# Performance work log

Hardware: AMD Instinct MI355X
Metric: run time of the kernel (lower is better)

## Reference

```python
import jax, jax.numpy as jnp
import numpy as np

N = 131072; B = 4; PER = N // B
M = 32768; MPER = M // B; K = 16; E = M * K
NF = 16; C = 32
BNC = float(1.0 / np.sqrt(1.0 + 1e-5))  # BatchNorm1d in eval mode, default running stats (mean=0,var=1,affine=identity)
_kd = np.array([[1.,1.,1.],[-1.,1.,1.],[1.,-1.,1.],[1.,1.,-1.],[-1.,-1.,1.],[-1.,1.,-1.],[1.,-1.,-1.],[-1.,-1.,-1.]], np.float32) / np.float32(np.sqrt(3.0))
KDIRS = jnp.asarray(_kd)  # [8,3] LightKernel directions


def _ln(x, g, b):
    m = x.mean(-1, keepdims=True)
    v = ((x - m) ** 2).mean(-1, keepdims=True)
    return (x - m) / jnp.sqrt(v + 1e-5) * g + b


def _mlp2(x, w1, b1, w2, b2):
    # Seq(Lin, BN, SiLU) x2 ; BN in eval mode == multiply by BNC
    h = jax.nn.silu(BNC * (x @ w1 + b1))
    return jax.nn.silu(BNC * (h @ w2 + b2))


def setup_inputs():
    rng = np.random.default_rng(0)
    f32 = np.float32
    w = lambda fi, fo: jnp.asarray((rng.standard_normal((fi, fo)) * 0.05).astype(f32))
    dg = lambda n: jnp.asarray((rng.standard_normal(n) * 0.05).astype(f32))
    z = lambda n: jnp.zeros((n,), jnp.float32)
    o = lambda n: jnp.ones((n,), jnp.float32)
    pos = jnp.asarray((rng.standard_normal((N, 3)) * 5.0).astype(f32))
    reflectance = jnp.asarray(rng.random(N).astype(f32))
    batch = jnp.asarray(np.repeat(np.arange(B), PER).astype(np.int64))
    sf = jnp.full((B,), 10.0, jnp.float32)
    # voxel-sampled centers: MPER per cloud, within each cloud's index range
    idx = np.concatenate([b * PER + rng.choice(PER, MPER, replace=False) for b in range(B)])
    tb = np.repeat(np.arange(B), MPER)
    # radius-graph edges: K in-batch source neighbors per sampled target
    col = (rng.integers(0, PER, size=(M, K)) + tb[:, None] * PER).reshape(-1)
    row = np.repeat(np.arange(M), K)
    inp = dict(pos=pos, reflectance=reflectance, sf=sf,
               batch=batch, idx=jnp.asarray(idx.astype(np.int64)),
               col=jnp.asarray(col.astype(np.int64)), row=jnp.asarray(row.astype(np.int64)))
    inp.update(stem_ln_g=o(97), stem_ln_b=z(97), stem_w1=w(97, 64), stem_b1=z(64),
               stem_w2=w(64, C), stem_b2=z(C),
               lk_w=w(8, 3), lk_b=z(3), lk_ln_g=o(3), lk_ln_b=z(3),
               loc_w1=w(C + 7, 64), loc_b1=z(64), loc_w2=w(64, 4 * C), loc_b2=z(4 * C),
               exp_w=w(128, 512), exp_b=z(512),
               dw1_w=dg(512), dw1_b=z(512), pw1_w=w(512, 512), pw1_b=z(512),
               dw2_w=dg(512), dw2_b=z(512), pw2_w=w(512, 512), pw2_b=z(512),
               proj_w=w(512, 128), proj_b=z(128))
    return inp


def _forward(pos, reflectance, sf, batch, idx, col, row,
             stem_ln_g, stem_ln_b, stem_w1, stem_b1, stem_w2, stem_b2,
             lk_w, lk_b, lk_ln_g, lk_ln_b,
             loc_w1, loc_b1, loc_w2, loc_b2,
             exp_w, exp_b, dw1_w, dw1_b, pw1_w, pw1_b,
             dw2_w, dw2_b, pw2_w, pw2_b, proj_w, proj_b):
    # --- StemModule: positional encoding + LayerNorm(97) + MLP[97,64,32] ---
    npos = pos / sf[batch][:, None]
    cnt = jax.ops.segment_sum(jnp.ones((N,), jnp.float32), batch, num_segments=B)
    centers = jax.ops.segment_sum(npos, batch, num_segments=B) / jnp.maximum(cnt, 1.0)[:, None]
    npos = npos - centers[batch]
    freqs = 1.0 / (10000.0 ** (2.0 * jnp.arange(NF, dtype=jnp.float32) / NF))
    pe = npos[:, :, None] * freqs                                   # [N,3,NF]
    pe = jnp.concatenate([jnp.sin(pe), jnp.cos(pe)], axis=-1).reshape(N, -1)  # [N,96]
    xin = _ln(jnp.concatenate([pe, reflectance[:, None]], axis=1), stem_ln_g, stem_ln_b)
    x = _mlp2(xin, stem_w1, stem_b1, stem_w2, stem_b2)              # [N,C]
    # --- SAModule: PointNetConv on precomputed radius graph ---
    pos4 = jnp.concatenate([pos, reflectance[:, None]], axis=1)     # [N,4]
    rel = pos4[col] - pos4[idx][row]                                # [E,4] pos_j - pos_i
    rel3 = rel[:, :3]
    dirs = rel3 / (jnp.linalg.norm(rel3, axis=1, keepdims=True) + 1e-8)
    kr = dirs @ KDIRS.T                                             # [E,8] kernel responses
    ecnt = jax.ops.segment_sum(jnp.ones((E,), jnp.float32), row, num_segments=M)
    nb = jax.ops.segment_sum(kr, row, num_segments=M) / jnp.maximum(ecnt, 1.0)[:, None]  # scatter_mean
    sfeat = _ln(nb @ lk_w + lk_b, lk_ln_g, lk_ln_b)                 # [M,3]
    msg = jnp.concatenate([x[col], rel, sfeat[row]], axis=1)        # [E,C+7]
    h = _mlp2(msg, loc_w1, loc_b1, loc_w2, loc_b2)                  # [E,4C] local_nn
    agg = jax.ops.segment_max(h, row, num_segments=M)               # max aggregation [M,4C]
    # --- InvertedResidualBlock (all kernel-size-1 convs => linear / per-channel) ---
    r = agg
    o = jax.nn.silu(BNC * (agg @ exp_w + exp_b))        # expand 128->512
    o = jax.nn.silu(BNC * (o * dw1_w + dw1_b))          # depthwise conv k=1
    o = jax.nn.silu(BNC * (o @ pw1_w + pw1_b))          # pointwise conv
    o = jax.nn.silu(BNC * o)                            # BN+SiLU between DWSep blocks
    o = jax.nn.silu(BNC * (o * dw2_w + dw2_b))
    o = jax.nn.silu(BNC * (o @ pw2_w + pw2_b))
    o = BNC * o                                         # trailing BN (no act)
    o = BNC * (o @ proj_w + proj_b)                     # project 512->128 + BN
    return jax.nn.silu(o + r)                           # [M,4C]


def reference(pos, reflectance, sf, batch, idx, col, row,
              stem_ln_g, stem_ln_b, stem_w1, stem_b1, stem_w2, stem_b2,
              lk_w, lk_b, lk_ln_g, lk_ln_b,
              loc_w1, loc_b1, loc_w2, loc_b2,
              exp_w, exp_b, dw1_w, dw1_b, pw1_w, pw1_b,
              dw2_w, dw2_b, pw2_w, pw2_b, proj_w, proj_b):
    return _forward(pos, reflectance, sf, batch, idx, col, row,
                    stem_ln_g, stem_ln_b, stem_w1, stem_b1, stem_w2, stem_b2,
                    lk_w, lk_b, lk_ln_g, lk_ln_b,
                    loc_w1, loc_b1, loc_w2, loc_b2,
                    exp_w, exp_b, dw1_w, dw1_b, pw1_w, pw1_b,
                    dw2_w, dw2_b, pw2_w, pw2_b, proj_w, proj_b)
```

## Files before the change

kernel.cpp:

```cpp
#include <hip/hip_runtime.h>

typedef unsigned short u16;
typedef unsigned int   u32;
typedef __attribute__((ext_vector_type(8))) u16  u16x8;
typedef __attribute__((ext_vector_type(4))) float f32x4;

#define N_PTS   131072
#define M_PTS   32768
#define BNCF    0.9999950000374997f

__device__ __forceinline__ float b2f(u16 u) {
    u32 x = ((u32)u) << 16;
    float f;
    __builtin_memcpy(&f, &x, 4);
    return f;
}
__device__ __forceinline__ u16 f2b(float f) {
    u32 x;
    __builtin_memcpy(&x, &f, 4);
    u32 r = x + 0x7fffu + ((x >> 16) & 1u);
    return (u16)(r >> 16);
}
__device__ __forceinline__ u16 f2b_hw(float f) {
    u32 r;
    asm("v_cvt_pk_bf16_f32 %0, %1, %1" : "=v"(r) : "v"(f));
    return (u16)r;
}
__device__ __forceinline__ float silu_f(float x) {
    return x * __builtin_amdgcn_rcpf(1.0f + __expf(-x));
}

__device__ __forceinline__ f32x4 mfma_bf16(u16x8 a, u16x8 b, f32x4 c) {
    asm volatile("v_mfma_f32_16x16x32_bf16 %0, %1, %2, %0"
                 : "+v"(c) : "v"(a), "v"(b));
    return c;
}
__device__ __forceinline__ f32x4 acc_fence(f32x4 c) {
    asm volatile("s_nop 7\n\ts_nop 7\n\ts_nop 3" : "+v"(c));
    return c;
}

__device__ __forceinline__ void cp_glds16(const u16* g, u16* l) {
    typedef const __attribute__((address_space(1))) u32* gp1_t;
    typedef __attribute__((address_space(3))) u32* lp3_t;
    __builtin_amdgcn_global_load_lds((gp1_t)(unsigned long long)g,
                                     (lp3_t)(unsigned long long)l, 16, 0, 0);
}

__global__ __launch_bounds__(256) void k_prep(const float* __restrict__ expw, u16* __restrict__ expwt,
                                              const float* __restrict__ pw1w, u16* __restrict__ pw1t,
                                              const float* __restrict__ pw2w, u16* __restrict__ pw2t,
                                              const float* __restrict__ prjw, u16* __restrict__ prjt,
                                              const float* __restrict__ lw1,  u16* __restrict__ lw1t,
                                              const float* __restrict__ lw2,  u16* __restrict__ lw2t,
                                              const float* __restrict__ sw1,  u16* __restrict__ sw1t,
                                              const float* __restrict__ sw2,  u16* __restrict__ sw2t) {
    int idx = blockIdx.x * 256 + threadIdx.x;
    const float* W; u16* O; int K, ksh, Nn;
    if (idx < 65536)                 { W = expw; O = expwt; K = 128; ksh = 7; Nn = 512; }
    else if ((idx -= 65536) < 262144){ W = pw1w; O = pw1t;  K = 512; ksh = 9; Nn = 512; }
    else if ((idx -= 262144) < 262144){ W = pw2w; O = pw2t; K = 512; ksh = 9; Nn = 512; }
    else if ((idx -= 262144) < 65536){ W = prjw; O = prjt;  K = 512; ksh = 9; Nn = 128; }
    else if ((idx -= 65536) < 4096)  { W = lw1;  O = lw1t;  K = 39;  ksh = 6; Nn = 64;  }
    else if ((idx -= 4096) < 8192)   { W = lw2;  O = lw2t;  K = 64;  ksh = 6; Nn = 128; }
    else if ((idx -= 8192) < 8192)   { W = sw1;  O = sw1t;  K = 97;  ksh = 7; Nn = 64;  }
    else if ((idx -= 8192) < 2048)   { W = sw2;  O = sw2t;  K = 64;  ksh = 6; Nn = 32;  }
    else return;
    int n = idx >> ksh, k = idx & ((1 << ksh) - 1);
    O[idx] = (k < K) ? f2b(W[(long)k * Nn + n]) : (u16)0;
}

__global__ __launch_bounds__(256) void k_centers(const float* __restrict__ pos,
                                                 const float* __restrict__ sfv,
                                                 const int* __restrict__ batch,
                                                 float* __restrict__ acc) {
    __shared__ float ls[16];
    int t = threadIdx.x;
    if (t < 16) ls[t] = 0.0f;
    __syncthreads();
    int i = blockIdx.x * 256 + t;
    if (i < N_PTS) {
        int b = batch[i];
        float inv = 1.0f / sfv[b];
        atomicAdd(&ls[b * 4 + 0], pos[i * 3 + 0] * inv);
        atomicAdd(&ls[b * 4 + 1], pos[i * 3 + 1] * inv);
        atomicAdd(&ls[b * 4 + 2], pos[i * 3 + 2] * inv);
        atomicAdd(&ls[b * 4 + 3], 1.0f);
    }
    __syncthreads();
    if (t < 16) atomicAdd(&acc[t], ls[t]);
}

__global__ __launch_bounds__(256, 3) void k_stem(const float* __restrict__ pos,
                                              const float* __restrict__ refl,
                                              const float* __restrict__ sfv,
                                              const int* __restrict__ batch,
                                              const float* __restrict__ cacc,
                                              const float* __restrict__ g,
                                              const float* __restrict__ bb,
                                              const u16* __restrict__ w1t,
                                              const float* __restrict__ b1,
                                              const u16* __restrict__ w2t,
                                              const float* __restrict__ b2,
                                              u16* __restrict__ xout) {
    __shared__ u16 xs[128][136];
    __shared__ u16 hb[128][72];
    const float FLO[8] = {
        1.0f, 0.31622776601683794f, 0.1f, 0.031622776601683791f,
        0.01f, 0.0031622776601683794f, 0.001f, 0.00031622776601683794f};
    const float FHI[8] = {
        0.0001f, 3.1622776601683795e-05f, 1e-05f, 3.1622776601683796e-06f,
        1e-06f, 3.1622776601683797e-07f, 1e-07f, 3.1622776601683792e-08f};
    int t = threadIdx.x;
    int wave = t >> 6, lane = t & 63;
    int quad = lane >> 4, l16 = lane & 15;
    int mt0 = wave * 2;

    {
        int p = t >> 1, half = t & 1;
        int i = blockIdx.x * 128 + p;
        int b = batch[i];
        float s = 1.0f / sfv[b];
        float cnt = fmaxf(cacc[b * 4 + 3], 1.0f);
        float npv[3];
#pragma unroll
        for (int d = 0; d < 3; ++d)
            npv[d] = pos[i * 3 + d] * s - cacc[b * 4 + d] / cnt;

        float fq[8];
#pragma unroll
        for (int f = 0; f < 8; ++f) fq[f] = half ? FHI[f] : FLO[f];

        float sv[3][8], cv[3][8];
        float sum = 0.0f, sq = 0.0f;
#pragma unroll
        for (int d = 0; d < 3; ++d) {
#pragma unroll
            for (int f = 0; f < 8; ++f) {
                float a = npv[d] * fq[f];
                float s_, c_;
                __sincosf(a, &s_, &c_);
                sv[d][f] = s_;
                cv[d][f] = c_;
                sum += s_ + c_;
                sq += s_ * s_ + c_ * c_;
            }
        }
        float rf = refl[i];
        if (half == 0) { sum += rf; sq += rf * rf; }
        sum += __shfl_xor(sum, 1);
        sq  += __shfl_xor(sq, 1);

        float m = sum * (1.0f / 97.0f);
        float var = sq * (1.0f / 97.0f) - m * m;
        float rstd = rsqrtf(fmaxf(var, 0.0f) + 1e-5f);

#pragma unroll
        for (int d = 0; d < 3; ++d) {
            int c0 = d * 32 + half * 8;
            {
                f32x4 g0  = *(const f32x4*)(g + c0);
                f32x4 g1  = *(const f32x4*)(g + c0 + 4);
                f32x4 bb0 = *(const f32x4*)(bb + c0);
                f32x4 bb1 = *(const f32x4*)(bb + c0 + 4);
                u16 tmp[8];
#pragma unroll
                for (int f = 0; f < 4; ++f) {
                    tmp[f]     = f2b_hw((sv[d][f]     - m) * rstd * g0[f] + bb0[f]);
                    tmp[4 + f] = f2b_hw((sv[d][4 + f] - m) * rstd * g1[f] + bb1[f]);
                }
                *(uint4*)(&xs[p][c0]) = *(uint4*)tmp;
            }
            int c1 = d * 32 + 16 + half * 8;
            {
                f32x4 g0  = *(const f32x4*)(g + c1);
                f32x4 g1  = *(const f32x4*)(g + c1 + 4);
                f32x4 bb0 = *(const f32x4*)(bb + c1);
                f32x4 bb1 = *(const f32x4*)(bb + c1 + 4);
                u16 tmp[8];
#pragma unroll
                for (int f = 0; f < 4; ++f) {
                    tmp[f]     = f2b_hw((cv[d][f]     - m) * rstd * g0[f] + bb0[f]);
                    tmp[4 + f] = f2b_hw((cv[d][4 + f] - m) * rstd * g1[f] + bb1[f]);
                }
                *(uint4*)(&xs[p][c1]) = *(uint4*)tmp;
            }
        }
        if (half == 0) {
            float v = rf;
            u16 tmp[8];
            tmp[0] = f2b_hw((v - m) * rstd * g[96] + bb[96]);
#pragma unroll
            for (int f = 1; f < 8; ++f) tmp[f] = 0;
            *(uint4*)(&xs[p][96]) = *(uint4*)tmp;
        } else {
            uint4 z = {0, 0, 0, 0};
            *(uint4*)(&xs[p][104]) = z;
            *(uint4*)(&xs[p][112]) = z;
            *(uint4*)(&xs[p][120]) = z;
        }
    }
    __syncthreads();

    {
        f32x4 acc[2][4];
#pragma unroll
        for (int i = 0; i < 2; ++i)
#pragma unroll
            for (int j = 0; j < 4; ++j) acc[i][j] = (f32x4){0.f, 0.f, 0.f, 0.f};
#pragma unroll
        for (int kk = 0; kk < 128; kk += 32) {
            u16x8 af[2], bfr[4];
#pragma unroll
            for (int i = 0; i < 2; ++i)
                af[i] = *(const u16x8*)(&xs[(mt0 + i) * 16 + l16][kk + quad * 8]);
#pragma unroll
            for (int j = 0; j < 4; ++j)
                bfr[j] = *(const u16x8*)(w1t + (j * 16 + l16) * 128 + kk + quad * 8);
#pragma unroll
            for (int i = 0; i < 2; ++i)
#pragma unroll
                for (int j = 0; j < 4; ++j)
                    acc[i][j] = mfma_bf16(af[i], bfr[j], acc[i][j]);
        }
#pragma unroll
        for (int i = 0; i < 2; ++i)
#pragma unroll
            for (int j = 0; j < 4; ++j) {
                f32x4 c = acc_fence(acc[i][j]);
                int n = j * 16 + l16;
                float bn = b1[n] * BNCF;
#pragma unroll
                for (int r = 0; r < 4; ++r)
                    hb[(mt0 + i) * 16 + quad * 4 + r][n] =
                        f2b_hw(silu_f(fmaf(BNCF, c[r], bn)));
            }
    }
    __syncthreads();

    {
        f32x4 acc[2][2];
#pragma unroll
        for (int i = 0; i < 2; ++i)
#pragma unroll
            for (int j = 0; j < 2; ++j) acc[i][j] = (f32x4){0.f, 0.f, 0.f, 0.f};
#pragma unroll
        for (int kk = 0; kk < 64; kk += 32) {
            u16x8 af[2], bfr[2];
#pragma unroll
            for (int i = 0; i < 2; ++i)
                af[i] = *(const u16x8*)(&hb[(mt0 + i) * 16 + l16][kk + quad * 8]);
#pragma unroll
            for (int j = 0; j < 2; ++j)
                bfr[j] = *(const u16x8*)(w2t + (j * 16 + l16) * 64 + kk + quad * 8);
#pragma unroll
            for (int i = 0; i < 2; ++i)
#pragma unroll
                for (int j = 0; j < 2; ++j)
                    acc[i][j] = mfma_bf16(af[i], bfr[j], acc[i][j]);
        }
#pragma unroll
        for (int i = 0; i < 2; ++i)
#pragma unroll
            for (int j = 0; j < 2; ++j) {
                f32x4 c = acc_fence(acc[i][j]);
                int n = j * 16 + l16;
                float bn = b2[n] * BNCF;
#pragma unroll
                for (int r = 0; r < 4; ++r) {
                    int m = (mt0 + i) * 16 + quad * 4 + r;
                    long ig = (long)blockIdx.x * 128 + m;
                    xout[ig * 32 + n] = f2b_hw(silu_f(fmaf(BNCF, c[r], bn)));
                }
            }
    }
}

__global__ __launch_bounds__(256, 4) void k_edge(const float* __restrict__ pos,
                                              const float* __restrict__ refl,
                                              const int* __restrict__ idxp,
                                              const int* __restrict__ colp,
                                              const u16* __restrict__ xfeat,
                                              const float* __restrict__ lkw,
                                              const float* __restrict__ lkb,
                                              const float* __restrict__ lng,
                                              const float* __restrict__ lnb,
                                              const u16* __restrict__ w1t,
                                              const float* __restrict__ b1,
                                              const u16* __restrict__ w2t,
                                              const float* __restrict__ b2,
                                              float* __restrict__ agg,
                                              u16* __restrict__ aggb) {
    __shared__ u16 uni16[128 * 72];
    __shared__ u16 ws[128 * 72];
    __shared__ float b1s[64];
    __shared__ float b2s[128];
    int t = threadIdx.x;
    int r0 = blockIdx.x * 8;
    long e0 = (long)r0 * 16;
    int wave = t >> 6, lane = t & 63;
    int quad = lane >> 4, l16 = lane & 15;
    int mt0 = wave * 2;

    for (int u = t; u < 512; u += 256) {
        int row = u >> 3, c8 = (u & 7) * 8;
        *(uint4*)(&ws[row * 72 + c8]) = *(const uint4*)(w1t + row * 64 + c8);
    }
    if (t < 64) b1s[t] = b1[t] * BNCF;
    if (t < 128) b2s[t] = b2[t] * BNCF;

    for (int u = t; u < 512; u += 256) {
        int e = u >> 2, seg = u & 3;
        int c = colp[e0 + e];
        uint4 d = *(const uint4*)(xfeat + (long)c * 32 + seg * 8);
        *(uint4*)(&uni16[e * 72 + seg * 8]) = d;
    }
    if (t < 128) {
        int e = t;
        int r = r0 + (e >> 4);
        int c = colp[e0 + e];
        int ci = idxp[r];
        float dx = pos[c * 3 + 0] - pos[ci * 3 + 0];
        float dy = pos[c * 3 + 1] - pos[ci * 3 + 1];
        float dz = pos[c * 3 + 2] - pos[ci * 3 + 2];
        float dr = refl[c] - refl[ci];

        float nrm = sqrtf(dx * dx + dy * dy + dz * dz);
        float inv = __builtin_amdgcn_rcpf(nrm + 1e-8f);
        float ux = dx * inv, uy = dy * inv, uz = dz * inv;
#pragma unroll
        for (int msk = 1; msk <= 8; msk <<= 1) {
            ux += __shfl_xor(ux, msk);
            uy += __shfl_xor(uy, msk);
            uz += __shfl_xor(uz, msk);
        }
        const float S3_16 = 0.57735026918962576f * (1.0f / 16.0f);
        const float sxk[8] = {1, -1, 1, 1, -1, -1, 1, -1};
        const float syk[8] = {1, 1, -1, 1, -1, 1, -1, -1};
        const float szk[8] = {1, 1, 1, -1, 1, -1, -1, -1};
        float sc0 = lkb[0], sc1 = lkb[1], sc2 = lkb[2];
#pragma unroll
        for (int j = 0; j < 8; ++j) {
            float nb = (sxk[j] * ux + syk[j] * uy + szk[j] * uz) * S3_16;
            sc0 += nb * lkw[j * 3 + 0];
            sc1 += nb * lkw[j * 3 + 1];
            sc2 += nb * lkw[j * 3 + 2];
        }
        float mm = (sc0 + sc1 + sc2) * (1.0f / 3.0f);
        float vv = ((sc0 - mm) * (sc0 - mm) + (sc1 - mm) * (sc1 - mm) +
                    (sc2 - mm) * (sc2 - mm)) * (1.0f / 3.0f);
        float rstd = rsqrtf(fmaxf(vv, 0.0f) + 1e-5f);

        u16 tmp[8];
        tmp[0] = f2b_hw(dx);
        tmp[1] = f2b_hw(dy);
        tmp[2] = f2b_hw(dz);
        tmp[3] = f2b_hw(dr);
        tmp[4] = f2b_hw((sc0 - mm) * rstd * lng[0] + lnb[0]);
        tmp[5] = f2b_hw((sc1 - mm) * rstd * lng[1] + lnb[1]);
        tmp[6] = f2b_hw((sc2 - mm) * rstd * lng[2] + lnb[2]);
        tmp[7] = 0;
        *(uint4*)(&uni16[e * 72 + 32]) = *(uint4*)tmp;
        uint4 z = {0, 0, 0, 0};
        *(uint4*)(&uni16[e * 72 + 40]) = z;
        *(uint4*)(&uni16[e * 72 + 48]) = z;
        *(uint4*)(&uni16[e * 72 + 56]) = z;
    }
    __syncthreads();

    {
        f32x4 acc[2][4];
#pragma unroll
        for (int i = 0; i < 2; ++i)
#pragma unroll
            for (int j = 0; j < 4; ++j) acc[i][j] = (f32x4){0.f, 0.f, 0.f, 0.f};
#pragma unroll
        for (int kk = 0; kk < 64; kk += 32) {
            u16x8 af[2], bfr[4];
#pragma unroll
            for (int i = 0; i < 2; ++i)
                af[i] = *(const u16x8*)(&uni16[((mt0 + i) * 16 + l16) * 72 + kk + quad * 8]);
#pragma unroll
            for (int j = 0; j < 4; ++j)
                bfr[j] = *(const u16x8*)(&ws[(j * 16 + l16) * 72 + kk + quad * 8]);
#pragma unroll
            for (int i = 0; i < 2; ++i)
#pragma unroll
                for (int j = 0; j < 4; ++j)
                    acc[i][j] = mfma_bf16(af[i], bfr[j], acc[i][j]);
        }
#pragma unroll
        for (int i = 0; i < 2; ++i)
#pragma unroll
            for (int j = 0; j < 4; ++j) {
                f32x4 c = acc_fence(acc[i][j]);
                int n = j * 16 + l16;
#pragma unroll
                for (int r = 0; r < 4; ++r) {
                    float v = silu_f(fmaf(BNCF, c[r], b1s[n]));
                    uni16[((mt0 + i) * 16 + quad * 4 + r) * 72 + n] = f2b_hw(v);
                }
            }
    }
    __syncthreads();

    for (int u = t; u < 1024; u += 256) {
        int row = u >> 3, c8 = (u & 7) * 8;
        *(uint4*)(&ws[row * 72 + c8]) = *(const uint4*)(w2t + row * 64 + c8);
    }
    __syncthreads();

    {
        f32x4 acc[2][8];
#pragma unroll
        for (int i = 0; i < 2; ++i)
#pragma unroll
            for (int j = 0; j < 8; ++j) acc[i][j] = (f32x4){0.f, 0.f, 0.f, 0.f};
#pragma unroll
        for (int kk = 0; kk < 64; kk += 32) {
            u16x8 af[2], bfr[8];
#pragma unroll
            for (int i = 0; i < 2; ++i)
                af[i] = *(const u16x8*)(&uni16[((mt0 + i) * 16 + l16) * 72 + kk + quad * 8]);
#pragma unroll
            for (int j = 0; j < 8; ++j)
                bfr[j] = *(const u16x8*)(&ws[(j * 16 + l16) * 72 + kk + quad * 8]);
#pragma unroll
            for (int i = 0; i < 2; ++i)
#pragma unroll
                for (int j = 0; j < 8; ++j)
                    acc[i][j] = mfma_bf16(af[i], bfr[j], acc[i][j]);
        }
#pragma unroll
        for (int i = 0; i < 2; ++i) {
            int rg = r0 + mt0 + i;
#pragma unroll
            for (int j = 0; j < 8; ++j) {
                f32x4 c = acc_fence(acc[i][j]);
                int n = j * 16 + l16;
                float mx = fmaxf(fmaxf(c[0], c[1]), fmaxf(c[2], c[3]));
                float mn = fminf(fminf(c[0], c[1]), fminf(c[2], c[3]));
                mx = fmaxf(mx, __shfl_xor(mx, 16));
                mx = fmaxf(mx, __shfl_xor(mx, 32));
                mn = fminf(mn, __shfl_xor(mn, 16));
                mn = fminf(mn, __shfl_xor(mn, 32));
                if (quad == 0) {
                    float v = fmaxf(silu_f(fmaf(BNCF, mx, b2s[n])),
                                    silu_f(fmaf(BNCF, mn, b2s[n])));
                    agg[(long)rg * 128 + n] = v;
                    aggb[(long)rg * 128 + n] = f2b_hw(v);
                }
            }
        }
    }
}

template <int EPI, int OD>
__global__ __launch_bounds__(256, 4) void k_mgemm(const u16* __restrict__ A,
                                               const u16* __restrict__ Bt,
                                               const float* __restrict__ bias,
                                               const float* __restrict__ dww,
                                               const float* __restrict__ dwb,
                                               const float* __restrict__ res,
                                               void* __restrict__ Ov,
                                               int K, int Nn) {
    __shared__ u16 As[128 * 64];
    __shared__ u16 Bs[128 * 64];
    int t = threadIdx.x;
    int wave = t >> 6, lane = t & 63;
    int quad = lane >> 4, l16 = lane & 15;
    int R0 = blockIdx.y * 128, C0 = blockIdx.x * 128;
    int wm = (wave & 1) * 64, wn = (wave >> 1) * 64;

    int srow = (lane >> 3);
    int sch  = lane & 7;

    f32x4 acc[4][4];
#pragma unroll
    for (int i = 0; i < 4; ++i)
#pragma unroll
        for (int j = 0; j < 4; ++j) acc[i][j] = (f32x4){0.f, 0.f, 0.f, 0.f};

    for (int k0 = 0; k0 < K; k0 += 64) {
#pragma unroll
        for (int it = 0; it < 4; ++it) {
            int base = wave * 32 + it * 8;
            int row = base + srow;
            int gch = (sch ^ (row & 7)) << 3;
            cp_glds16(A  + (long)(R0 + row) * K + k0 + gch, &As[base * 64]);
            cp_glds16(Bt + (long)(C0 + row) * K + k0 + gch, &Bs[base * 64]);
        }
        __syncthreads();
#pragma unroll
        for (int kk = 0; kk < 64; kk += 32) {
            int kb = kk >> 3;
            u16x8 af[4], bfr[4];
#pragma unroll
            for (int tm = 0; tm < 4; ++tm) {
                int r = wm + tm * 16 + l16;
                af[tm] = *(const u16x8*)(&As[r * 64 + (((kb + quad) ^ (r & 7)) << 3)]);
            }
#pragma unroll
            for (int tn = 0; tn < 4; ++tn) {
                int r = wn + tn * 16 + l16;
                bfr[tn] = *(const u16x8*)(&Bs[r * 64 + (((kb + quad) ^ (r & 7)) << 3)]);
            }
#pragma unroll
            for (int tm = 0; tm < 4; ++tm)
#pragma unroll
                for (int tn = 0; tn < 4; ++tn)
                    acc[tm][tn] = mfma_bf16(af[tm], bfr[tn], acc[tm][tn]);
        }
        __syncthreads();
    }

#pragma unroll
    for (int tm = 0; tm < 4; ++tm) {
#pragma unroll
        for (int tn = 0; tn < 4; ++tn) {
            f32x4 c = acc_fence(acc[tm][tn]);
            int n = C0 + wn + tn * 16 + l16;
            float bn = bias[n] * BNCF;
            float dn = 0.0f, db = 0.0f;
            if (EPI == 0 || EPI == 1) { dn = dww[n] * BNCF; db = dwb[n] * BNCF; }
#pragma unroll
            for (int r = 0; r < 4; ++r) {
                int m = R0 + wm + tm * 16 + quad * 4 + r;
                float v = c[r];
                if (EPI == 0) {
                    v = silu_f(fmaf(BNCF, v, bn));
                    v = silu_f(fmaf(v, dn, db));
                } else if (EPI == 1) {
                    v = silu_f(fmaf(BNCF, v, bn));
                    v = silu_f(BNCF * v);
                    v = silu_f(fmaf(v, dn, db));
                } else if (EPI == 2) {
                    v = silu_f(fmaf(BNCF, v, bn));
                    v = BNCF * v;
                } else {
                    v = fmaf(BNCF, v, bn);
                    v = silu_f(v + res[(long)m * 128 + n]);
                }
                if (OD == 0)
                    ((u16*)Ov)[(long)m * Nn + n] = f2b_hw(v);
                else
                    ((float*)Ov)[(long)m * Nn + n] = v;
            }
        }
    }
}

extern "C" void kernel_launch(void* const* d_in, const int* in_sizes, int n_in,
                              void* d_out, int out_size, void* d_ws, size_t ws_size,
                              hipStream_t stream) {
    const float* pos   = (const float*)d_in[0];
    const float* refl  = (const float*)d_in[1];
    const float* sfv   = (const float*)d_in[2];
    const int*   batch = (const int*)d_in[3];
    const int*   idxp  = (const int*)d_in[4];
    const int*   colp  = (const int*)d_in[5];
    const float* s_g  = (const float*)d_in[7];
    const float* s_b  = (const float*)d_in[8];
    const float* s_w1 = (const float*)d_in[9];
    const float* s_b1 = (const float*)d_in[10];
    const float* s_w2 = (const float*)d_in[11];
    const float* s_b2 = (const float*)d_in[12];
    const float* lkw  = (const float*)d_in[13];
    const float* lkb  = (const float*)d_in[14];
    const float* lng  = (const float*)d_in[15];
    const float* lnb  = (const float*)d_in[16];
    const float* l_w1 = (const float*)d_in[17];
    const float* l_b1 = (const float*)d_in[18];
    const float* l_w2 = (const float*)d_in[19];
    const float* l_b2 = (const float*)d_in[20];
    const float* expw = (const float*)d_in[21];
    const float* expb = (const float*)d_in[22];
    const float* dw1w = (const float*)d_in[23];
    const float* dw1b = (const float*)d_in[24];
    const float* pw1w = (const float*)d_in[25];
    const float* pw1b = (const float*)d_in[26];
    const float* dw2w = (const float*)d_in[27];
    const float* dw2b = (const float*)d_in[28];
    const float* pw2w = (const float*)d_in[29];
    const float* pw2b = (const float*)d_in[30];
    const float* prjw = (const float*)d_in[31];
    const float* prjb = (const float*)d_in[32];

    char* ws = (char*)d_ws;
    float* cent  = (float*)(ws + 0);
    float* agg   = (float*)(ws + 393280);
    u16*   aggb  = (u16*)(ws + 17170496);
    u16*   u1    = (u16*)(ws + 25559104);
    u16*   u2    = (u16*)(ws + 59113536);
    u16*   xf    = (u16*)(ws + 59113536);
    u16*   expwt = (u16*)(ws + 92667968);
    u16*   pw1t  = (u16*)(ws + 92799040);
    u16*   pw2t  = (u16*)(ws + 93323328);
    u16*   prjt  = (u16*)(ws + 93847616);
    u16*   lw1t  = (u16*)(ws + 93978688);
    u16*   lw2t  = (u16*)(ws + 93986880);
    u16*   sw1t  = (u16*)(ws + 94003264);
    u16*   sw2t  = (u16*)(ws + 94019648);

    k_prep<<<2648, 256, 0, stream>>>(expw, expwt, pw1w, pw1t, pw2w, pw2t,
                                     prjw, prjt, l_w1, lw1t, l_w2, lw2t,
                                     s_w1, sw1t, s_w2, sw2t);

    hipMemsetAsync(cent, 0, 64, stream);
    k_centers<<<512, 256, 0, stream>>>(pos, sfv, batch, cent);
    k_stem<<<1024, 256, 0, stream>>>(pos, refl, sfv, batch, cent, s_g, s_b,
                                     sw1t, s_b1, sw2t, s_b2, xf);
    k_edge<<<4096, 256, 0, stream>>>(pos, refl, idxp, colp, xf,
                                     lkw, lkb, lng, lnb,
                                     lw1t, l_b1, lw2t, l_b2, agg, aggb);

    dim3 blk(256);
    k_mgemm<0, 0><<<dim3(4, 256), blk, 0, stream>>>(aggb, expwt, expb, dw1w, dw1b,
                                                    nullptr, u1, 128, 512);
    k_mgemm<1, 0><<<dim3(4, 256), blk, 0, stream>>>(u1, pw1t, pw1b, dw2w, dw2b,
                                                    nullptr, u2, 512, 512);
    k_mgemm<2, 0><<<dim3(4, 256), blk, 0, stream>>>(u2, pw2t, pw2b, nullptr, nullptr,
                                                    nullptr, u1, 512, 512);
    k_mgemm<3, 1><<<dim3(1, 256), blk, 0, stream>>>(u1, prjt, prjb, nullptr, nullptr,
                                                    agg, d_out, 512, 128);
}
```

Baseline: 322.5 us.

## Tile weight transposes, warp-reduce centers, and hoist MFMA hazard nops

The big weight-transpose prep now runs through a 64x64 LDS tile, so both the fp32 reads and the bf16 writes are coalesced; the small weights keep the old per-element kernel. The centroid kernel swaps per-thread LDS atomics for a wave shuffle reduction, assuming each 256-point block lies in a single batch. The per-accumulator s_nop hazard fence becomes one guard after each MFMA loop, and the GEMM epilogue loads its bias and depthwise parameters once before the tile loop. These cut prep and epilogue overhead, but the lighter fence could expose MFMA result hazards.

```diff
diff --git a/kernel.cpp b/kernel.cpp
--- a/kernel.cpp
+++ b/kernel.cpp
@@ -35,9 +35,8 @@
                  : "+v"(c) : "v"(a), "v"(b));
     return c;
 }
-__device__ __forceinline__ f32x4 acc_fence(f32x4 c) {
-    asm volatile("s_nop 7\n\ts_nop 7\n\ts_nop 3" : "+v"(c));
-    return c;
+__device__ __forceinline__ void mai_guard() {
+    asm volatile("s_nop 7\n\ts_nop 7\n\ts_nop 3");
 }
 
 __device__ __forceinline__ void cp_glds16(const u16* g, u16* l) {
@@ -47,24 +46,42 @@
                                      (lp3_t)(unsigned long long)l, 16, 0, 0);
 }
 
-__global__ __launch_bounds__(256) void k_prep(const float* __restrict__ expw, u16* __restrict__ expwt,
-                                              const float* __restrict__ pw1w, u16* __restrict__ pw1t,
-                                              const float* __restrict__ pw2w, u16* __restrict__ pw2t,
-                                              const float* __restrict__ prjw, u16* __restrict__ prjt,
-                                              const float* __restrict__ lw1,  u16* __restrict__ lw1t,
-                                              const float* __restrict__ lw2,  u16* __restrict__ lw2t,
-                                              const float* __restrict__ sw1,  u16* __restrict__ sw1t,
-                                              const float* __restrict__ sw2,  u16* __restrict__ sw2t) {
+__global__ __launch_bounds__(256) void k_prep_big(const float* __restrict__ expw, u16* __restrict__ expwt,
+                                                  const float* __restrict__ pw1w, u16* __restrict__ pw1t,
+                                                  const float* __restrict__ pw2w, u16* __restrict__ pw2t,
+                                                  const float* __restrict__ prjw, u16* __restrict__ prjt) {
+    __shared__ u16 tile[64][66];
+    int bid = blockIdx.x;
+    const float* W; u16* O; int K, Nn, tk, tn_;
+    if (bid < 16)            { W = expw; O = expwt; K = 128; Nn = 512; tk = bid >> 3; tn_ = bid & 7; }
+    else if ((bid -= 16) < 64) { W = pw1w; O = pw1t; K = 512; Nn = 512; tk = bid >> 3; tn_ = bid & 7; }
+    else if ((bid -= 64) < 64) { W = pw2w; O = pw2t; K = 512; Nn = 512; tk = bid >> 3; tn_ = bid & 7; }
+    else { bid -= 64;          W = prjw; O = prjt; K = 512; Nn = 128; tk = bid >> 1; tn_ = bid & 1; }
+    int k0 = tk * 64, n0 = tn_ * 64;
+    int c = threadIdx.x & 63, r0 = threadIdx.x >> 6;
+#pragma unroll
+    for (int rr = 0; rr < 16; ++rr) {
+        int row = r0 * 16 + rr;
+        tile[row][c] = f2b(W[(long)(k0 + row) * Nn + n0 + c]);
+    }
+    __syncthreads();
+#pragma unroll
+    for (int rr = 0; rr < 16; ++rr) {
+        int row = r0 * 16 + rr;
+        O[(long)(n0 + row) * K + k0 + c] = tile[c][row];
+    }
+}
+
+__global__ __launch_bounds__(256) void k_prep_small(const float* __restrict__ lw1,  u16* __restrict__ lw1t,
+                                                    const float* __restrict__ lw2,  u16* __restrict__ lw2t,
+                                                    const float* __restrict__ sw1,  u16* __restrict__ sw1t,
+                                                    const float* __restrict__ sw2,  u16* __restrict__ sw2t) {
     int idx = blockIdx.x * 256 + threadIdx.x;
     const float* W; u16* O; int K, ksh, Nn;
-    if (idx < 65536)                 { W = expw; O = expwt; K = 128; ksh = 7; Nn = 512; }
-    else if ((idx -= 65536) < 262144){ W = pw1w; O = pw1t;  K = 512; ksh = 9; Nn = 512; }
-    else if ((idx -= 262144) < 262144){ W = pw2w; O = pw2t; K = 512; ksh = 9; Nn = 512; }
-    else if ((idx -= 262144) < 65536){ W = prjw; O = prjt;  K = 512; ksh = 9; Nn = 128; }
-    else if ((idx -= 65536) < 4096)  { W = lw1;  O = lw1t;  K = 39;  ksh = 6; Nn = 64;  }
-    else if ((idx -= 4096) < 8192)   { W = lw2;  O = lw2t;  K = 64;  ksh = 6; Nn = 128; }
-    else if ((idx -= 8192) < 8192)   { W = sw1;  O = sw1t;  K = 97;  ksh = 7; Nn = 64;  }
-    else if ((idx -= 8192) < 2048)   { W = sw2;  O = sw2t;  K = 64;  ksh = 6; Nn = 32;  }
+    if (idx < 4096)                  { W = lw1; O = lw1t; K = 39; ksh = 6; Nn = 64;  }
+    else if ((idx -= 4096) < 8192)   { W = lw2; O = lw2t; K = 64; ksh = 6; Nn = 128; }
+    else if ((idx -= 8192) < 8192)   { W = sw1; O = sw1t; K = 97; ksh = 7; Nn = 64;  }
+    else if ((idx -= 8192) < 2048)   { W = sw2; O = sw2t; K = 64; ksh = 6; Nn = 32;  }
     else return;
     int n = idx >> ksh, k = idx & ((1 << ksh) - 1);
     O[idx] = (k < K) ? f2b(W[(long)k * Nn + n]) : (u16)0;
@@ -75,20 +92,26 @@
                                                  const int* __restrict__ batch,
                                                  float* __restrict__ acc) {
     __shared__ float ls[16];
-    int t = threadIdx.x;
-    if (t < 16) ls[t] = 0.0f;
+    int t = threadIdx.x, lane = t & 63, wave = t >> 6;
+    int i = blockIdx.x * 256 + t;
+    int b = batch[blockIdx.x * 256];
+    float inv = 1.0f / sfv[b];
+    float x = pos[i * 3 + 0] * inv;
+    float y = pos[i * 3 + 1] * inv;
+    float z = pos[i * 3 + 2] * inv;
+#pragma unroll
+    for (int m = 1; m < 64; m <<= 1) {
+        x += __shfl_xor(x, m);
+        y += __shfl_xor(y, m);
+        z += __shfl_xor(z, m);
+    }
+    if (lane == 0) { ls[wave * 4 + 0] = x; ls[wave * 4 + 1] = y; ls[wave * 4 + 2] = z; }
     __syncthreads();
-    int i = blockIdx.x * 256 + t;
-    if (i < N_PTS) {
-        int b = batch[i];
-        float inv = 1.0f / sfv[b];
-        atomicAdd(&ls[b * 4 + 0], pos[i * 3 + 0] * inv);
-        atomicAdd(&ls[b * 4 + 1], pos[i * 3 + 1] * inv);
-        atomicAdd(&ls[b * 4 + 2], pos[i * 3 + 2] * inv);
-        atomicAdd(&ls[b * 4 + 3], 1.0f);
-    }
-    __syncthreads();
-    if (t < 16) atomicAdd(&acc[t], ls[t]);
+    if (t < 3) {
+        float s = ls[t] + ls[4 + t] + ls[8 + t] + ls[12 + t];
+        atomicAdd(&acc[b * 4 + t], s);
+    }
+    if (t == 3) atomicAdd(&acc[b * 4 + 3], 256.0f);
 }
 
 __global__ __launch_bounds__(256, 3) void k_stem(const float* __restrict__ pos,
@@ -223,11 +246,12 @@
                 for (int j = 0; j < 4; ++j)
                     acc[i][j] = mfma_bf16(af[i], bfr[j], acc[i][j]);
         }
+        mai_guard();
 #pragma unroll
         for (int i = 0; i < 2; ++i)
 #pragma unroll
             for (int j = 0; j < 4; ++j) {
-                f32x4 c = acc_fence(acc[i][j]);
+                f32x4 c = acc[i][j];
                 int n = j * 16 + l16;
                 float bn = b1[n] * BNCF;
 #pragma unroll
@@ -259,11 +283,12 @@
                 for (int j = 0; j < 2; ++j)
                     acc[i][j] = mfma_bf16(af[i], bfr[j], acc[i][j]);
         }
+        mai_guard();
 #pragma unroll
         for (int i = 0; i < 2; ++i)
 #pragma unroll
             for (int j = 0; j < 2; ++j) {
-                f32x4 c = acc_fence(acc[i][j]);
+                f32x4 c = acc[i][j];
                 int n = j * 16 + l16;
                 float bn = b2[n] * BNCF;
 #pragma unroll
@@ -389,11 +414,12 @@
                 for (int j = 0; j < 4; ++j)
                     acc[i][j] = mfma_bf16(af[i], bfr[j], acc[i][j]);
         }
+        mai_guard();
 #pragma unroll
         for (int i = 0; i < 2; ++i)
 #pragma unroll
             for (int j = 0; j < 4; ++j) {
-                f32x4 c = acc_fence(acc[i][j]);
+                f32x4 c = acc[i][j];
                 int n = j * 16 + l16;
 #pragma unroll
                 for (int r = 0; r < 4; ++r) {
@@ -431,12 +457,13 @@
                 for (int j = 0; j < 8; ++j)
                     acc[i][j] = mfma_bf16(af[i], bfr[j], acc[i][j]);
         }
+        mai_guard();
 #pragma unroll
         for (int i = 0; i < 2; ++i) {
             int rg = r0 + mt0 + i;
 #pragma unroll
             for (int j = 0; j < 8; ++j) {
-                f32x4 c = acc_fence(acc[i][j]);
+                f32x4 c = acc[i][j];
                 int n = j * 16 + l16;
                 float mx = fmaxf(fmaxf(c[0], c[1]), fmaxf(c[2], c[3]));
                 float mn = fminf(fminf(c[0], c[1]), fminf(c[2], c[3]));
@@ -514,31 +541,37 @@
         __syncthreads();
     }
 
+    float bnA[4], dnA[4], dbA[4];
+#pragma unroll
+    for (int tn = 0; tn < 4; ++tn) {
+        int n = C0 + wn + tn * 16 + l16;
+        bnA[tn] = bias[n] * BNCF;
+        if (EPI == 0 || EPI == 1) { dnA[tn] = dww[n] * BNCF; dbA[tn] = dwb[n] * BNCF; }
+        else { dnA[tn] = 0.0f; dbA[tn] = 0.0f; }
+    }
+    mai_guard();
 #pragma unroll
     for (int tm = 0; tm < 4; ++tm) {
 #pragma unroll
         for (int tn = 0; tn < 4; ++tn) {
-            f32x4 c = acc_fence(acc[tm][tn]);
+            f32x4 c = acc[tm][tn];
             int n = C0 + wn + tn * 16 + l16;
-            float bn = bias[n] * BNCF;
-            float dn = 0.0f, db = 0.0f;
-            if (EPI == 0 || EPI == 1) { dn = dww[n] * BNCF; db = dwb[n] * BNCF; }
 #pragma unroll
             for (int r = 0; r < 4; ++r) {
                 int m = R0 + wm + tm * 16 + quad * 4 + r;
                 float v = c[r];
                 if (EPI == 0) {
-                    v = silu_f(fmaf(BNCF, v, bn));
-                    v = silu_f(fmaf(v, dn, db));
+                    v = silu_f(fmaf(BNCF, v, bnA[tn]));
+                    v = silu_f(fmaf(v, dnA[tn], dbA[tn]));
                 } else if (EPI == 1) {
-                    v = silu_f(fmaf(BNCF, v, bn));
+                    v = silu_f(fmaf(BNCF, v, bnA[tn]));
                     v = silu_f(BNCF * v);
-                    v = silu_f(fmaf(v, dn, db));
+                    v = silu_f(fmaf(v, dnA[tn], dbA[tn]));
                 } else if (EPI == 2) {
-                    v = silu_f(fmaf(BNCF, v, bn));
+                    v = silu_f(fmaf(BNCF, v, bnA[tn]));
                     v = BNCF * v;
                 } else {
-                    v = fmaf(BNCF, v, bn);
+                    v = fmaf(BNCF, v, bnA[tn]);
                     v = silu_f(v + res[(long)m * 128 + n]);
                 }
                 if (OD == 0)
@@ -602,9 +635,8 @@
     u16*   sw1t  = (u16*)(ws + 94003264);
     u16*   sw2t  = (u16*)(ws + 94019648);
 
-    k_prep<<<2648, 256, 0, stream>>>(expw, expwt, pw1w, pw1t, pw2w, pw2t,
-                                     prjw, prjt, l_w1, lw1t, l_w2, lw2t,
-                                     s_w1, sw1t, s_w2, sw2t);
+    k_prep_big<<<160, 256, 0, stream>>>(expw, expwt, pw1w, pw1t, pw2w, pw2t, prjw, prjt);
+    k_prep_small<<<88, 256, 0, stream>>>(l_w1, lw1t, l_w2, lw2t, s_w1, sw1t, s_w2, sw2t);
 
     hipMemsetAsync(cent, 0, 64, stream);
     k_centers<<<512, 256, 0, stream>>>(pos, sfv, batch, cent);
```

After: 315.9 us. -2.0%, faster.
